# Kernel tuning notes

Hardware: AMD Instinct MI355X
Metric: run time of the kernel (lower is better)

Reference implementation:

```python
import jax, jax.numpy as jnp
import numpy as np

GS = 128          # r_group_size
Q_MAX = 7.0       # 2**(q_bits-1)-1, q_bits=4
R_MAX = 7.0       # 2**(r_bits-1)-1, r_bits=4
R_MIN = -8.0      # -R_MAX-1
EPS = 1e-8


def _fake_quant_group(w, n_bits=4, group_size=128, eps=1e-8):
    # symmetric group-wise fake quant of the weight (done once at __init__)
    qmax = 2 ** (n_bits - 1) - 1
    qmin = -qmax - 1
    O, I = w.shape
    wg = w.reshape(O, I // group_size, group_size)
    scale = jnp.maximum(jnp.max(jnp.abs(wg), axis=-1, keepdims=True) / qmax, eps)
    wq = jnp.clip(jnp.round(wg / scale), qmin, qmax) * scale
    return wq.reshape(O, I)


def _select_pow2_base(t):
    # smallest value in {2,4,8,16,32,64} that is >= t (64 if none)
    base = jnp.full_like(t, 64.0)
    for v in (32.0, 16.0, 8.0, 4.0, 2.0):
        base = jnp.where(t <= v, jnp.full_like(t, v), base)
    return base


def setup_inputs() -> dict:
    key = jax.random.key(0)
    kx, kw, kb = jax.random.split(key, 3)
    B, S, IN, OUT = 4, 2048, 4096, 11008
    x = jax.random.normal(kx, (B, S, IN), dtype=jnp.float32)
    w_raw = jax.random.normal(kw, (OUT, IN), dtype=jnp.float32)
    weight = _fake_quant_group(w_raw, n_bits=4, group_size=128)
    bias = jax.random.normal(kb, (OUT,), dtype=jnp.float32)
    return {"x": x, "weight": weight, "bias": bias}


def reference(x, weight, bias):
    # dynamic quotient-remainder activation fake-quant (init path)
    H = x.shape[-1]
    xg = x.astype(jnp.float32).reshape(x.shape[:-1] + (H // GS, GS))  # [..., G, gs]
    max_abs = jnp.maximum(jnp.max(jnp.abs(xg), axis=-1, keepdims=True), EPS)
    base = _select_pow2_base(max_abs / Q_MAX)                 # [..., G, 1]
    q = jnp.clip(jnp.round(xg / base), -Q_MAX, Q_MAX)          # quotient
    r = xg - base * q                                          # remainder
    max_abs_r = jnp.maximum(jnp.max(jnp.abs(r), axis=-1, keepdims=True), EPS)
    scale_r = max_abs_r / R_MAX
    r_dq = jnp.clip(jnp.round(r / scale_r), R_MIN, R_MAX) * scale_r
    x_recon = (base * q + r_dq).reshape(x.shape)
    # F.linear: y = x @ W^T + b
    return jnp.einsum("bsi,oi->bso", x_recon, weight) + bias
```

## Files before the change

### kernel.cpp

```cpp
#include <hip/hip_runtime.h>
#include <stdint.h>
#include <stddef.h>

typedef __bf16 bf16x8 __attribute__((ext_vector_type(8)));
typedef float  f32x4  __attribute__((ext_vector_type(4)));
typedef float  f32x2  __attribute__((ext_vector_type(2)));

__device__ __forceinline__ unsigned short f2bf(float f) {
  unsigned int u = __builtin_bit_cast(unsigned int, f);
  u += 0x7fffu + ((u >> 16) & 1u);
  return (unsigned short)(u >> 16);
}

__device__ __forceinline__ void gld_lds16(const void* g, void* l) {
  __builtin_amdgcn_global_load_lds(
      (__attribute__((address_space(1))) void*)(g),
      (__attribute__((address_space(3))) void*)(l), 16, 0, 0);
}

#define BAR()     asm volatile("s_barrier" ::: "memory")
#define WAITVM(n) asm volatile("s_waitcnt vmcnt(" #n ")" ::: "memory")
#define WAITLG0() asm volatile("s_waitcnt lgkmcnt(0)" ::: "memory")
#define SCHED0()  __builtin_amdgcn_sched_barrier(0)

__global__ __launch_bounds__(256) void quant_x_kernel(
    const float* __restrict__ x, unsigned short* __restrict__ xb, long long ngroups)
{
  const int lane = threadIdx.x & 63;
  const int wv   = threadIdx.x >> 6;
  long long g = (long long)blockIdx.x * 4 + wv;
  if (g >= ngroups) return;

  const float* xg = x + g * 128;
  f32x2 v = __builtin_nontemporal_load(
      reinterpret_cast<const f32x2*>(xg + lane * 2));

  float m = fmaxf(fabsf(v[0]), fabsf(v[1]));
  #pragma unroll
  for (int off = 32; off; off >>= 1) m = fmaxf(m, __shfl_xor(m, off));
  m = fmaxf(m, 1e-8f);

  float t = m / 7.0f;
  float base = t <= 2.f ? 2.f : t <= 4.f ? 4.f : t <= 8.f ? 8.f
             : t <= 16.f ? 16.f : t <= 32.f ? 32.f : 64.f;
  float inv_base = 1.0f / base;

  float q0 = fminf(fmaxf(rintf(v[0] * inv_base), -7.f), 7.f);
  float q1 = fminf(fmaxf(rintf(v[1] * inv_base), -7.f), 7.f);
  float r0 = v[0] - base * q0;
  float r1 = v[1] - base * q1;

  float mr = fmaxf(fabsf(r0), fabsf(r1));
  #pragma unroll
  for (int off = 32; off; off >>= 1) mr = fmaxf(mr, __shfl_xor(mr, off));
  mr = fmaxf(mr, 1e-8f);
  float scale_r = mr / 7.0f;

  float rd0 = fminf(fmaxf(rintf(r0 / scale_r), -8.f), 7.f) * scale_r;
  float rd1 = fminf(fmaxf(rintf(r1 / scale_r), -8.f), 7.f) * scale_r;

  float y0 = base * q0 + rd0;
  float y1 = base * q1 + rd1;

  unsigned int packed = (unsigned int)f2bf(y0) | ((unsigned int)f2bf(y1) << 16);
  *reinterpret_cast<unsigned int*>(xb + g * 128 + lane * 2) = packed;
}

__global__ __launch_bounds__(256) void cvt_w_kernel(
    const float* __restrict__ w, unsigned short* __restrict__ wb, long long n)
{
  long long i = ((long long)blockIdx.x * blockDim.x + threadIdx.x) * 8;
  if (i + 7 >= n) {
    if (i >= n) return;
    for (long long j = i; j < n; ++j) wb[j] = f2bf(w[j]);
    return;
  }
  f32x4 v0 = __builtin_nontemporal_load(reinterpret_cast<const f32x4*>(w + i));
  f32x4 v1 = __builtin_nontemporal_load(reinterpret_cast<const f32x4*>(w + i + 4));
  uint4 o;
  o.x = (unsigned)f2bf(v0[0]) | ((unsigned)f2bf(v0[1]) << 16);
  o.y = (unsigned)f2bf(v0[2]) | ((unsigned)f2bf(v0[3]) << 16);
  o.z = (unsigned)f2bf(v1[0]) | ((unsigned)f2bf(v1[1]) << 16);
  o.w = (unsigned)f2bf(v1[2]) | ((unsigned)f2bf(v1[3]) << 16);
  *reinterpret_cast<uint4*>(wb + i) = o;
}

#define BM 256
#define BN 256
#define BK 64

#define MFMA16(a, b, c) __builtin_amdgcn_mfma_f32_16x16x32_bf16(a, b, c, 0, 0, 0)

__global__ __launch_bounds__(512, 2) void gemm256_bias(
    const unsigned short* __restrict__ A,
    const unsigned short* __restrict__ B,
    const float* __restrict__ bias,
    float* __restrict__ C,
    int M, int N, int K)
{
  __shared__ unsigned short lds[2][2][2][128 * 64];

  const int tid  = threadIdx.x;
  const int lane = tid & 63;
  const int wid  = tid >> 6;
  const int wm   = wid >> 2;
  const int wn   = wid & 3;
  const int laneq = lane & 15;
  const int laneh = lane >> 4;
  const int lq7   = laneq & 7;

  const int ntm = M / BM;
  const int ntn = N / BN;
  int tm, tn;
  if ((ntm & 15) == 0) {
    int rem = blockIdx.x;
    int str = 0, stc = 0, w = 16;
    for (;;) {
      int w2 = (ntn - stc * 16 < 16) ? (ntn - stc * 16) : 16;
      int sz = 16 * w2;
      if (rem < sz) { w = w2; break; }
      rem -= sz;
      ++stc;
      if (stc * 16 >= ntn) { stc = 0; ++str; }
    }
    tm = str * 16 + rem / w;
    tn = stc * 16 + rem % w;
  } else {
    tm = (int)blockIdx.x / ntn;
    tn = (int)blockIdx.x % ntn;
  }
  const size_t m0 = (size_t)tm * BM;
  const size_t n0 = (size_t)tn * BN;

  const int NT = K / BK;

  const int ss0 = (laneh ^ lq7);
  const int ss1 = ((4 + laneh) ^ lq7);

  const char* ldsb = (const char*)&lds[0][0][0][0];
  const int aOff = wm * 16384 + laneq * 128;
  const int bOff = 32768 + (wn >> 1) * 16384 + ((wn & 1) * 64 + laneq) * 128;

  const int c0 = tid, c1 = 512 + tid;
  const int r0 = c0 >> 3, sl0 = (c0 & 7) ^ (r0 & 7);
  const int r1 = c1 >> 3, sl1 = (c1 & 7) ^ (r1 & 7);
  const unsigned short* gA0 = A + (m0 + r0) * (size_t)K + sl0 * 8;
  const unsigned short* gA1 = A + (m0 + r1) * (size_t)K + sl1 * 8;
  const unsigned short* gB0 = B + (n0 + r0) * (size_t)K + sl0 * 8;
  const unsigned short* gB1 = B + (n0 + r1) * (size_t)K + sl1 * 8;
  const size_t hstep = (size_t)128 * K;

  char* dst0 = (char*)ldsb + wid * 1024;
  char* dst1 = dst0 + 65536;

  f32x4 acc[8][4];
  #pragma unroll
  for (int i = 0; i < 8; i++)
    #pragma unroll
    for (int j = 0; j < 4; j++)
      acc[i][j] = (f32x4){0.f, 0.f, 0.f, 0.f};

  #define STAGE(mat, h, kt, dstD)                                            \
    do {                                                                     \
      const unsigned short* g0_ = (mat == 0) ? gA0 : gB0;                    \
      const unsigned short* g1_ = (mat == 0) ? gA1 : gB1;                    \
      gld_lds16(g0_ + (size_t)(h) * hstep + (size_t)(kt) * 64,               \
                (dstD) + (mat) * 32768 + (h) * 16384);                       \
      gld_lds16(g1_ + (size_t)(h) * hstep + (size_t)(kt) * 64,               \
                (dstD) + (mat) * 32768 + (h) * 16384 + 8192);                \
    } while (0)

  STAGE(0, 0, 0, dst0); STAGE(0, 1, 0, dst0);
  STAGE(1, 0, 0, dst0); STAGE(1, 1, 0, dst0);
  STAGE(0, 0, 1, dst1); STAGE(0, 1, 1, dst1);
  STAGE(1, 0, 1, dst1); STAGE(1, 1, 1, dst1);
  WAITVM(8);
  BAR();

  bf16x8 al[4][2], ah[4][2], bl[2][2], bh[2][2];

  for (int t = 0; t < NT; ++t) {
    const int d = t & 1;
    const char* aS0 = ldsb + (d << 16) + aOff + ss0 * 16;
    const char* aS1 = ldsb + (d << 16) + aOff + ss1 * 16;
    const char* bS0 = ldsb + (d << 16) + bOff + ss0 * 16;
    const char* bS1 = ldsb + (d << 16) + bOff + ss1 * 16;
    char* dstn = d ? dst1 : dst0;

    #pragma unroll
    for (int mi = 0; mi < 4; ++mi) {
      al[mi][0] = *(const bf16x8*)(aS0 + mi * 2048);
      al[mi][1] = *(const bf16x8*)(aS1 + mi * 2048);
    }
    #pragma unroll
    for (int nj = 0; nj < 2; ++nj) {
      bl[nj][0] = *(const bf16x8*)(bS0 + nj * 2048);
      bl[nj][1] = *(const bf16x8*)(bS1 + nj * 2048);
    }
    BAR();
    WAITLG0(); SCHED0();
    __builtin_amdgcn_s_setprio(1);
    #pragma unroll
    for (int mi = 0; mi < 4; ++mi)
      #pragma unroll
      for (int nj = 0; nj < 2; ++nj) {
        acc[mi][nj] = MFMA16(al[mi][0], bl[nj][0], acc[mi][nj]);
        acc[mi][nj] = MFMA16(al[mi][1], bl[nj][1], acc[mi][nj]);
      }
    __builtin_amdgcn_s_setprio(0);

    #pragma unroll
    for (int nj = 0; nj < 2; ++nj) {
      bh[nj][0] = *(const bf16x8*)(bS0 + 4096 + nj * 2048);
      bh[nj][1] = *(const bf16x8*)(bS1 + 4096 + nj * 2048);
    }
    BAR();
    WAITLG0(); SCHED0();
    __builtin_amdgcn_s_setprio(1);
    #pragma unroll
    for (int mi = 0; mi < 4; ++mi)
      #pragma unroll
      for (int nj = 0; nj < 2; ++nj) {
        acc[mi][2 + nj] = MFMA16(al[mi][0], bh[nj][0], acc[mi][2 + nj]);
        acc[mi][2 + nj] = MFMA16(al[mi][1], bh[nj][1], acc[mi][2 + nj]);
      }
    __builtin_amdgcn_s_setprio(0);

    #pragma unroll
    for (int mi = 0; mi < 4; ++mi) {
      ah[mi][0] = *(const bf16x8*)(aS0 + 8192 + mi * 2048);
      ah[mi][1] = *(const bf16x8*)(aS1 + 8192 + mi * 2048);
    }
    BAR();
    if (t + 2 < NT) { STAGE(1, 0, t + 2, dstn); STAGE(1, 1, t + 2, dstn); }
    WAITLG0(); SCHED0();
    __builtin_amdgcn_s_setprio(1);
    #pragma unroll
    for (int mi = 0; mi < 4; ++mi)
      #pragma unroll
      for (int nj = 0; nj < 2; ++nj) {
        acc[4 + mi][2 + nj] = MFMA16(ah[mi][0], bh[nj][0], acc[4 + mi][2 + nj]);
        acc[4 + mi][2 + nj] = MFMA16(ah[mi][1], bh[nj][1], acc[4 + mi][2 + nj]);
      }
    __builtin_amdgcn_s_setprio(0);

    BAR();
    if (t + 2 < NT) { STAGE(0, 0, t + 2, dstn); STAGE(0, 1, t + 2, dstn); }
    SCHED0();
    __builtin_amdgcn_s_setprio(1);
    #pragma unroll
    for (int mi = 0; mi < 4; ++mi)
      #pragma unroll
      for (int nj = 0; nj < 2; ++nj) {
        acc[4 + mi][nj] = MFMA16(ah[mi][0], bl[nj][0], acc[4 + mi][nj]);
        acc[4 + mi][nj] = MFMA16(ah[mi][1], bl[nj][1], acc[4 + mi][nj]);
      }
    __builtin_amdgcn_s_setprio(0);
    if (t == NT - 2)      { WAITVM(0); }
    else if (t < NT - 2)  { WAITVM(8); }
    BAR();
  }
  #undef STAGE

  #pragma unroll
  for (int nj = 0; nj < 4; ++nj) {
    int col = (int)n0 + wn * 64 + nj * 16 + laneq;
    float bv = bias[col];
    #pragma unroll
    for (int mi = 0; mi < 8; ++mi) {
      size_t row = m0 + wm * 128 + mi * 16 + laneh * 4;
      float* cp = C + row * (size_t)N + col;
      #pragma unroll
      for (int r = 0; r < 4; ++r)
        __builtin_nontemporal_store(acc[mi][nj][r] + bv, cp + (size_t)r * N);
    }
  }
}

extern "C" void kernel_launch(void* const* d_in, const int* in_sizes, int n_in,
                              void* d_out, int out_size, void* d_ws, size_t ws_size,
                              hipStream_t stream) {
  const float* x    = (const float*)d_in[0];
  const float* w    = (const float*)d_in[1];
  const float* bias = (const float*)d_in[2];
  float* out = (float*)d_out;

  const long long xN = in_sizes[0];
  const long long wN = in_sizes[1];
  const int N = in_sizes[2];
  const int K = (int)(wN / N);
  const int M = (int)(xN / K);

  unsigned short* xb = (unsigned short*)d_ws;
  unsigned short* wb = xb + xN;

  long long ngroups = xN / 128;
  long long qblocks = (ngroups + 3) / 4;
  quant_x_kernel<<<(int)qblocks, 256, 0, stream>>>(x, xb, ngroups);

  long long cblocks = (wN + 2047) / 2048;
  cvt_w_kernel<<<(int)cblocks, 256, 0, stream>>>(w, wb, wN);

  int grid = (M / BM) * (N / BN);
  gemm256_bias<<<grid, 512, 0, stream>>>(xb, wb, bias, out, M, N, K);
}
```

Before: 782.2 us.

## Restructure GEMM main loop into simple prefetch-next-tile double buffering

Replaces the four-phase interleaved schedule, which prefetched two tiles ahead with barriers between MFMA quarters, with a simpler loop. Each iteration issues the global-to-LDS loads for tile t+1 at the top, reads all LDS fragments, runs all MFMAs in one block, then waits for all outstanding loads and barriers once. This removes several barriers and lgkmcnt waits per iteration. In exchange, prefetch depth drops from two tiles to one, so each iteration fully drains its memory loads, and the LDS reads and MFMAs are no longer interleaved.

```diff
diff --git a/kernel.cpp b/kernel.cpp
--- a/kernel.cpp
+++ b/kernel.cpp
@@ -20,7 +20,6 @@
 
 #define BAR()     asm volatile("s_barrier" ::: "memory")
 #define WAITVM(n) asm volatile("s_waitcnt vmcnt(" #n ")" ::: "memory")
-#define WAITLG0() asm volatile("s_waitcnt lgkmcnt(0)" ::: "memory")
 #define SCHED0()  __builtin_amdgcn_sched_barrier(0)
 
 __global__ __launch_bounds__(256) void quant_x_kernel(
@@ -160,21 +159,20 @@
     for (int j = 0; j < 4; j++)
       acc[i][j] = (f32x4){0.f, 0.f, 0.f, 0.f};
 
-  #define STAGE(mat, h, kt, dstD)                                            \
+  #define STAGETILE(kt, dstD)                                                \
     do {                                                                     \
-      const unsigned short* g0_ = (mat == 0) ? gA0 : gB0;                    \
-      const unsigned short* g1_ = (mat == 0) ? gA1 : gB1;                    \
-      gld_lds16(g0_ + (size_t)(h) * hstep + (size_t)(kt) * 64,               \
-                (dstD) + (mat) * 32768 + (h) * 16384);                       \
-      gld_lds16(g1_ + (size_t)(h) * hstep + (size_t)(kt) * 64,               \
-                (dstD) + (mat) * 32768 + (h) * 16384 + 8192);                \
+      gld_lds16(gA0 + (size_t)(kt) * 64,          (dstD));                   \
+      gld_lds16(gA1 + (size_t)(kt) * 64,          (dstD) + 8192);            \
+      gld_lds16(gA0 + hstep + (size_t)(kt) * 64,  (dstD) + 16384);           \
+      gld_lds16(gA1 + hstep + (size_t)(kt) * 64,  (dstD) + 16384 + 8192);    \
+      gld_lds16(gB0 + (size_t)(kt) * 64,          (dstD) + 32768);           \
+      gld_lds16(gB1 + (size_t)(kt) * 64,          (dstD) + 32768 + 8192);    \
+      gld_lds16(gB0 + hstep + (size_t)(kt) * 64,  (dstD) + 49152);           \
+      gld_lds16(gB1 + hstep + (size_t)(kt) * 64,  (dstD) + 49152 + 8192);    \
     } while (0)
 
-  STAGE(0, 0, 0, dst0); STAGE(0, 1, 0, dst0);
-  STAGE(1, 0, 0, dst0); STAGE(1, 1, 0, dst0);
-  STAGE(0, 0, 1, dst1); STAGE(0, 1, 1, dst1);
-  STAGE(1, 0, 1, dst1); STAGE(1, 1, 1, dst1);
-  WAITVM(8);
+  STAGETILE(0, dst0);
+  WAITVM(0);
   BAR();
 
   bf16x8 al[4][2], ah[4][2], bl[2][2], bh[2][2];
@@ -185,7 +183,8 @@
     const char* aS1 = ldsb + (d << 16) + aOff + ss1 * 16;
     const char* bS0 = ldsb + (d << 16) + bOff + ss0 * 16;
     const char* bS1 = ldsb + (d << 16) + bOff + ss1 * 16;
-    char* dstn = d ? dst1 : dst0;
+
+    if (t + 1 < NT) { char* dn = d ? dst0 : dst1; STAGETILE(t + 1, dn); }
 
     #pragma unroll
     for (int mi = 0; mi < 4; ++mi) {
@@ -197,44 +196,35 @@
       bl[nj][0] = *(const bf16x8*)(bS0 + nj * 2048);
       bl[nj][1] = *(const bf16x8*)(bS1 + nj * 2048);
     }
-    BAR();
-    WAITLG0(); SCHED0();
-    __builtin_amdgcn_s_setprio(1);
-    #pragma unroll
-    for (int mi = 0; mi < 4; ++mi)
-      #pragma unroll
-      for (int nj = 0; nj < 2; ++nj) {
-        acc[mi][nj] = MFMA16(al[mi][0], bl[nj][0], acc[mi][nj]);
-        acc[mi][nj] = MFMA16(al[mi][1], bl[nj][1], acc[mi][nj]);
-      }
-    __builtin_amdgcn_s_setprio(0);
-
     #pragma unroll
     for (int nj = 0; nj < 2; ++nj) {
       bh[nj][0] = *(const bf16x8*)(bS0 + 4096 + nj * 2048);
       bh[nj][1] = *(const bf16x8*)(bS1 + 4096 + nj * 2048);
     }
-    BAR();
-    WAITLG0(); SCHED0();
-    __builtin_amdgcn_s_setprio(1);
-    #pragma unroll
-    for (int mi = 0; mi < 4; ++mi)
-      #pragma unroll
-      for (int nj = 0; nj < 2; ++nj) {
-        acc[mi][2 + nj] = MFMA16(al[mi][0], bh[nj][0], acc[mi][2 + nj]);
-        acc[mi][2 + nj] = MFMA16(al[mi][1], bh[nj][1], acc[mi][2 + nj]);
-      }
-    __builtin_amdgcn_s_setprio(0);
-
     #pragma unroll
     for (int mi = 0; mi < 4; ++mi) {
       ah[mi][0] = *(const bf16x8*)(aS0 + 8192 + mi * 2048);
       ah[mi][1] = *(const bf16x8*)(aS1 + 8192 + mi * 2048);
     }
-    BAR();
-    if (t + 2 < NT) { STAGE(1, 0, t + 2, dstn); STAGE(1, 1, t + 2, dstn); }
-    WAITLG0(); SCHED0();
+    SCHED0();
+
     __builtin_amdgcn_s_setprio(1);
+    #pragma unroll
+    for (int mi = 0; mi < 4; ++mi)
+      #pragma unroll
+      for (int nj = 0; nj < 2; ++nj) {
+        acc[mi][nj] = MFMA16(al[mi][0], bl[nj][0], acc[mi][nj]);
+        acc[mi][nj] = MFMA16(al[mi][1], bl[nj][1], acc[mi][nj]);
+      }
+    SCHED0();
+    #pragma unroll
+    for (int mi = 0; mi < 4; ++mi)
+      #pragma unroll
+      for (int nj = 0; nj < 2; ++nj) {
+        acc[mi][2 + nj] = MFMA16(al[mi][0], bh[nj][0], acc[mi][2 + nj]);
+        acc[mi][2 + nj] = MFMA16(al[mi][1], bh[nj][1], acc[mi][2 + nj]);
+      }
+    SCHED0();
     #pragma unroll
     for (int mi = 0; mi < 4; ++mi)
       #pragma unroll
@@ -242,12 +232,6 @@
         acc[4 + mi][2 + nj] = MFMA16(ah[mi][0], bh[nj][0], acc[4 + mi][2 + nj]);
         acc[4 + mi][2 + nj] = MFMA16(ah[mi][1], bh[nj][1], acc[4 + mi][2 + nj]);
       }
-    __builtin_amdgcn_s_setprio(0);
-
-    BAR();
-    if (t + 2 < NT) { STAGE(0, 0, t + 2, dstn); STAGE(0, 1, t + 2, dstn); }
-    SCHED0();
-    __builtin_amdgcn_s_setprio(1);
     #pragma unroll
     for (int mi = 0; mi < 4; ++mi)
       #pragma unroll
@@ -256,11 +240,11 @@
         acc[4 + mi][nj] = MFMA16(ah[mi][1], bl[nj][1], acc[4 + mi][nj]);
       }
     __builtin_amdgcn_s_setprio(0);
-    if (t == NT - 2)      { WAITVM(0); }
-    else if (t < NT - 2)  { WAITVM(8); }
+
+    WAITVM(0);
     BAR();
   }
-  #undef STAGE
+  #undef STAGETILE
 
   #pragma unroll
   for (int nj = 0; nj < 4; ++nj) {
```

After: 763.3 us. 2.4% less time.
